# Kernel optimization log

Hardware: AMD Instinct MI355X
Metric: run time of the kernel (lower is better)

The kernel has to match this reference:

```python
import jax, jax.numpy as jnp
import numpy as np

EPS = 0.1
N_ITERS = 20


def setup_inputs() -> dict:
    key = jax.random.key(0)
    D = jax.random.uniform(key, (32, 1024, 1024), dtype=jnp.float32)
    return {"D": D}


def reference(D) -> jnp.ndarray:
    log_K0 = -D / EPS  # [B, N, M]

    def body(_, log_K):
        # row normalization (over dim 2), then column normalization (over dim 1)
        log_K = log_K - jax.scipy.special.logsumexp(log_K, axis=2, keepdims=True)
        log_K = log_K - jax.scipy.special.logsumexp(log_K, axis=1, keepdims=True)
        return log_K

    log_K = jax.lax.fori_loop(0, N_ITERS, body, log_K0)
    # transport plan weighted cost, summed per batch, then mean over batch
    return jnp.mean(jnp.sum(jnp.exp(log_K) * D, axis=(1, 2)))
```

## Files before the change

kernel.cpp:

```cpp
#include <hip/hip_runtime.h>

#define BATCH 32
#define NMAT 1024
#define NPB 64
#define RPB (NMAT / NPB)
#define NBLOCKS (BATCH * NPB)
#define N_ITERS 20
#define SHIFT 5.0f

typedef _Float16 h8 __attribute__((ext_vector_type(8)));

__device__ __forceinline__ float wave_allsum(float s) {
#pragma unroll
    for (int off = 1; off < 64; off <<= 1) s += __shfl_xor(s, off, 64);
    return s;
}

__device__ __forceinline__ float4 f4add(float4 a, float4 b) {
    return make_float4(a.x + b.x, a.y + b.y, a.z + b.z, a.w + b.w);
}

__global__ __launch_bounds__(256) void pass1_build(const float* __restrict__ D,
                                                   _Float16* __restrict__ E,
                                                   float* __restrict__ P) {
    const int j = blockIdx.x;
    const int row0 = j * RPB;
    const int wave = threadIdx.x >> 6, lane = threadIdx.x & 63;

    float4 acc[4] = {make_float4(0,0,0,0), make_float4(0,0,0,0),
                     make_float4(0,0,0,0), make_float4(0,0,0,0)};

#pragma unroll
    for (int i = 0; i < RPB / 4; ++i) {
        const int r = row0 + wave + (i << 2);
        const float4* Dr = (const float4*)(D + ((size_t)r << 10));
        h8* Er = (h8*)(E + ((size_t)r << 10));
        float t[16];
        float s = 0.f;
#pragma unroll
        for (int k2 = 0; k2 < 2; ++k2) {
            const int c = lane + (k2 << 6);
            float4 d0 = Dr[2 * c], d1 = Dr[2 * c + 1];
            float* tv = t + (k2 << 3);
            tv[0] = __expf(fmaf(d0.x, -10.f, SHIFT));
            tv[1] = __expf(fmaf(d0.y, -10.f, SHIFT));
            tv[2] = __expf(fmaf(d0.z, -10.f, SHIFT));
            tv[3] = __expf(fmaf(d0.w, -10.f, SHIFT));
            tv[4] = __expf(fmaf(d1.x, -10.f, SHIFT));
            tv[5] = __expf(fmaf(d1.y, -10.f, SHIFT));
            tv[6] = __expf(fmaf(d1.z, -10.f, SHIFT));
            tv[7] = __expf(fmaf(d1.w, -10.f, SHIFT));
            h8 o;
#pragma unroll
            for (int q = 0; q < 8; ++q) o[q] = (_Float16)tv[q];
            Er[c] = o;
#pragma unroll
            for (int q = 0; q < 8; ++q) s += tv[q];
        }
        s = wave_allsum(s);
        const float rs = __builtin_amdgcn_rcpf(s);
#pragma unroll
        for (int k2 = 0; k2 < 2; ++k2) {
            float* tv = t + (k2 << 3);
            float4* a0 = &acc[k2 << 1];
            a0[0].x = fmaf(tv[0], rs, a0[0].x);
            a0[0].y = fmaf(tv[1], rs, a0[0].y);
            a0[0].z = fmaf(tv[2], rs, a0[0].z);
            a0[0].w = fmaf(tv[3], rs, a0[0].w);
            a0[1].x = fmaf(tv[4], rs, a0[1].x);
            a0[1].y = fmaf(tv[5], rs, a0[1].y);
            a0[1].z = fmaf(tv[6], rs, a0[1].z);
            a0[1].w = fmaf(tv[7], rs, a0[1].w);
        }
    }

    __shared__ float4 pc[4][256];
#pragma unroll
    for (int k2 = 0; k2 < 2; ++k2) {
        const int c = lane + (k2 << 6);
        pc[wave][2 * c]     = acc[k2 << 1];
        pc[wave][2 * c + 1] = acc[(k2 << 1) + 1];
    }
    __syncthreads();
    const int i = threadIdx.x;
    float4 o = f4add(f4add(pc[0][i], pc[1][i]), f4add(pc[2][i], pc[3][i]));
    ((float4*)(P + ((size_t)j << 10)))[i] = o;
}

template <bool LAST>
__global__ __launch_bounds__(256) void pass_iter(const _Float16* __restrict__ E,
                                                 const float* __restrict__ ev_in,
                                                 float* __restrict__ P,
                                                 float* __restrict__ Q,
                                                 float* __restrict__ out) {
    const int j = blockIdx.x;
    const int row0 = j * RPB;
    const int b = row0 >> 10;
    const int wave = threadIdx.x >> 6, lane = threadIdx.x & 63;

    float ev[16];
    {
        const float4* evb = (const float4*)(ev_in + (b << 10));
#pragma unroll
        for (int k2 = 0; k2 < 2; ++k2) {
            const int c = lane + (k2 << 6);
            float4 e0 = evb[2 * c], e1 = evb[2 * c + 1];
            float* e = ev + (k2 << 3);
            e[0] = e0.x; e[1] = e0.y; e[2] = e0.z; e[3] = e0.w;
            e[4] = e1.x; e[5] = e1.y; e[6] = e1.z; e[7] = e1.w;
        }
    }

    float4 acc[4] = {make_float4(0,0,0,0), make_float4(0,0,0,0),
                     make_float4(0,0,0,0), make_float4(0,0,0,0)};
    float4 qacc[4] = {make_float4(0,0,0,0), make_float4(0,0,0,0),
                      make_float4(0,0,0,0), make_float4(0,0,0,0)};

#pragma unroll
    for (int i = 0; i < RPB / 4; ++i) {
        const int r = row0 + wave + (i << 2);
        const h8* Er = (const h8*)(E + ((size_t)r << 10));
        h8 h0 = Er[lane], h1 = Er[lane + 64];
        float t[16];
#pragma unroll
        for (int q = 0; q < 8; ++q) { t[q] = (float)h0[q]; t[8 + q] = (float)h1[q]; }
        float s = 0.f;
#pragma unroll
        for (int q = 0; q < 16; ++q) s = fmaf(t[q], ev[q], s);
        s = wave_allsum(s);
        const float rs = __builtin_amdgcn_rcpf(s);
#pragma unroll
        for (int k2 = 0; k2 < 2; ++k2) {
            float* tv = t + (k2 << 3);
            float4* a0 = &acc[k2 << 1];
            a0[0].x = fmaf(tv[0], rs, a0[0].x);
            a0[0].y = fmaf(tv[1], rs, a0[0].y);
            a0[0].z = fmaf(tv[2], rs, a0[0].z);
            a0[0].w = fmaf(tv[3], rs, a0[0].w);
            a0[1].x = fmaf(tv[4], rs, a0[1].x);
            a0[1].y = fmaf(tv[5], rs, a0[1].y);
            a0[1].z = fmaf(tv[6], rs, a0[1].z);
            a0[1].w = fmaf(tv[7], rs, a0[1].w);
        }
        if (LAST) {
#pragma unroll
            for (int k2 = 0; k2 < 2; ++k2) {
                float* tv = t + (k2 << 3);
                float4* q0 = &qacc[k2 << 1];
                float w[8];
#pragma unroll
                for (int q = 0; q < 8; ++q) {
                    const float d = (SHIFT - __logf(tv[q])) * 0.1f;
                    w[q] = tv[q] * d;
                }
                q0[0].x = fmaf(w[0], rs, q0[0].x);
                q0[0].y = fmaf(w[1], rs, q0[0].y);
                q0[0].z = fmaf(w[2], rs, q0[0].z);
                q0[0].w = fmaf(w[3], rs, q0[0].w);
                q0[1].x = fmaf(w[4], rs, q0[1].x);
                q0[1].y = fmaf(w[5], rs, q0[1].y);
                q0[1].z = fmaf(w[6], rs, q0[1].z);
                q0[1].w = fmaf(w[7], rs, q0[1].w);
            }
        }
    }

    __shared__ float4 pc[4][256];
#pragma unroll
    for (int k2 = 0; k2 < 2; ++k2) {
        const int c = lane + (k2 << 6);
        pc[wave][2 * c]     = acc[k2 << 1];
        pc[wave][2 * c + 1] = acc[(k2 << 1) + 1];
    }
    __syncthreads();
    {
        const int i = threadIdx.x;
        float4 o = f4add(f4add(pc[0][i], pc[1][i]), f4add(pc[2][i], pc[3][i]));
        ((float4*)(P + ((size_t)j << 10)))[i] = o;
    }
    if (LAST) {
        __syncthreads();
#pragma unroll
        for (int k2 = 0; k2 < 2; ++k2) {
            const int c = lane + (k2 << 6);
            pc[wave][2 * c]     = qacc[k2 << 1];
            pc[wave][2 * c + 1] = qacc[(k2 << 1) + 1];
        }
        __syncthreads();
        const int i = threadIdx.x;
        float4 o = f4add(f4add(pc[0][i], pc[1][i]), f4add(pc[2][i], pc[3][i]));
        ((float4*)(Q + ((size_t)j << 10)))[i] = o;
        if (j == 0 && threadIdx.x == 0) out[0] = 0.f;
    }
}

__global__ __launch_bounds__(256) void reduce_ev(const float* __restrict__ P,
                                                 float* __restrict__ ev) {
    int g = blockIdx.x * 256 + threadIdx.x;
    int b = g >> 10, m = g & 1023;
    const float* Pb = P + (((size_t)b * NPB) << 10) + m;
    float s = 0.f;
#pragma unroll 8
    for (int jj = 0; jj < NPB; ++jj) s += Pb[(size_t)jj << 10];
    ev[g] = 1.0f / s;
}

__global__ __launch_bounds__(256) void loss_final(const float* __restrict__ P,
                                                  const float* __restrict__ Q,
                                                  float* __restrict__ out) {
    int g = blockIdx.x * 256 + threadIdx.x;
    int b = g >> 10, m = g & 1023;
    const float* Pb = P + (((size_t)b * NPB) << 10) + m;
    const float* Qb = Q + (((size_t)b * NPB) << 10) + m;
    float s = 0.f, q = 0.f;
#pragma unroll 8
    for (int jj = 0; jj < NPB; ++jj) {
        s += Pb[(size_t)jj << 10];
        q += Qb[(size_t)jj << 10];
    }
    float c = q / s;
    c = wave_allsum(c);
    __shared__ float sm[4];
    int wave = threadIdx.x >> 6, lane = threadIdx.x & 63;
    if (lane == 0) sm[wave] = c;
    __syncthreads();
    if (threadIdx.x == 0)
        atomicAdd(out, (sm[0] + sm[1] + sm[2] + sm[3]) * (1.0f / (float)BATCH));
}

extern "C" void kernel_launch(void* const* d_in, const int* in_sizes, int n_in,
                              void* d_out, int out_size, void* d_ws, size_t ws_size,
                              hipStream_t stream) {
    const float* D = (const float*)d_in[0];
    float* out = (float*)d_out;

    float* ev = (float*)d_ws;
    float* P  = ev + BATCH * NMAT;
    float* Q  = P + (size_t)NBLOCKS * NMAT;
    _Float16* E = (_Float16*)(Q + (size_t)NBLOCKS * NMAT);

    pass1_build<<<NBLOCKS, 256, 0, stream>>>(D, E, P);
    for (int t = 1; t < N_ITERS - 1; ++t) {
        reduce_ev<<<(BATCH * NMAT) / 256, 256, 0, stream>>>(P, ev);
        pass_iter<false><<<NBLOCKS, 256, 0, stream>>>(E, ev, P, Q, out);
    }
    reduce_ev<<<(BATCH * NMAT) / 256, 256, 0, stream>>>(P, ev);
    pass_iter<true><<<NBLOCKS, 256, 0, stream>>>(E, ev, P, Q, out);
    loss_final<<<(BATCH * NMAT) / 256, 256, 0, stream>>>(P, Q, out);
}
```

Before: 560.1 us.

## Fuse Sinkhorn iterations into persistent kernel with on-chip E and grid barriers

Replaces the per-iteration launches of pass_iter and reduce_ev with one persistent kernel of 256 blocks of 1024 threads. Each block keeps its 128-row slab of the fp16 kernel matrix on chip, five rows per wave in registers and three in LDS, so the matrix is not re-read from HBM each iteration. Iterations are separated by atomic-counter grid barriers, and column scalings are reduced from double-buffered partials. The risks are register and LDS pressure, a deadlock if all 256 blocks are not co-resident, and the cost of the barrier spins.

```diff
diff --git a/kernel.cpp b/kernel.cpp
--- a/kernel.cpp
+++ b/kernel.cpp
@@ -2,9 +2,11 @@
 
 #define BATCH 32
 #define NMAT 1024
-#define NPB 64
-#define RPB (NMAT / NPB)
-#define NBLOCKS (BATCH * NPB)
+#define NBLK 256
+#define NWAVE 16
+#define ROWS_PW 8
+#define REG_ROWS 5
+#define LDS_ROWS 3
 #define N_ITERS 20
 #define SHIFT 5.0f
 
@@ -20,212 +22,196 @@
     return make_float4(a.x + b.x, a.y + b.y, a.z + b.z, a.w + b.w);
 }
 
-__global__ __launch_bounds__(256) void pass1_build(const float* __restrict__ D,
-                                                   _Float16* __restrict__ E,
-                                                   float* __restrict__ P) {
-    const int j = blockIdx.x;
-    const int row0 = j * RPB;
-    const int wave = threadIdx.x >> 6, lane = threadIdx.x & 63;
-
-    float4 acc[4] = {make_float4(0,0,0,0), make_float4(0,0,0,0),
-                     make_float4(0,0,0,0), make_float4(0,0,0,0)};
-
-#pragma unroll
-    for (int i = 0; i < RPB / 4; ++i) {
-        const int r = row0 + wave + (i << 2);
-        const float4* Dr = (const float4*)(D + ((size_t)r << 10));
-        h8* Er = (h8*)(E + ((size_t)r << 10));
-        float t[16];
-        float s = 0.f;
-#pragma unroll
-        for (int k2 = 0; k2 < 2; ++k2) {
-            const int c = lane + (k2 << 6);
-            float4 d0 = Dr[2 * c], d1 = Dr[2 * c + 1];
-            float* tv = t + (k2 << 3);
-            tv[0] = __expf(fmaf(d0.x, -10.f, SHIFT));
-            tv[1] = __expf(fmaf(d0.y, -10.f, SHIFT));
-            tv[2] = __expf(fmaf(d0.z, -10.f, SHIFT));
-            tv[3] = __expf(fmaf(d0.w, -10.f, SHIFT));
-            tv[4] = __expf(fmaf(d1.x, -10.f, SHIFT));
-            tv[5] = __expf(fmaf(d1.y, -10.f, SHIFT));
-            tv[6] = __expf(fmaf(d1.z, -10.f, SHIFT));
-            tv[7] = __expf(fmaf(d1.w, -10.f, SHIFT));
-            h8 o;
-#pragma unroll
-            for (int q = 0; q < 8; ++q) o[q] = (_Float16)tv[q];
-            Er[c] = o;
-#pragma unroll
-            for (int q = 0; q < 8; ++q) s += tv[q];
-        }
-        s = wave_allsum(s);
-        const float rs = __builtin_amdgcn_rcpf(s);
-#pragma unroll
-        for (int k2 = 0; k2 < 2; ++k2) {
-            float* tv = t + (k2 << 3);
-            float4* a0 = &acc[k2 << 1];
-            a0[0].x = fmaf(tv[0], rs, a0[0].x);
-            a0[0].y = fmaf(tv[1], rs, a0[0].y);
-            a0[0].z = fmaf(tv[2], rs, a0[0].z);
-            a0[0].w = fmaf(tv[3], rs, a0[0].w);
-            a0[1].x = fmaf(tv[4], rs, a0[1].x);
-            a0[1].y = fmaf(tv[5], rs, a0[1].y);
-            a0[1].z = fmaf(tv[6], rs, a0[1].z);
-            a0[1].w = fmaf(tv[7], rs, a0[1].w);
-        }
-    }
-
-    __shared__ float4 pc[4][256];
-#pragma unroll
-    for (int k2 = 0; k2 < 2; ++k2) {
-        const int c = lane + (k2 << 6);
-        pc[wave][2 * c]     = acc[k2 << 1];
-        pc[wave][2 * c + 1] = acc[(k2 << 1) + 1];
-    }
-    __syncthreads();
-    const int i = threadIdx.x;
-    float4 o = f4add(f4add(pc[0][i], pc[1][i]), f4add(pc[2][i], pc[3][i]));
-    ((float4*)(P + ((size_t)j << 10)))[i] = o;
-}
-
-template <bool LAST>
-__global__ __launch_bounds__(256) void pass_iter(const _Float16* __restrict__ E,
-                                                 const float* __restrict__ ev_in,
-                                                 float* __restrict__ P,
-                                                 float* __restrict__ Q,
-                                                 float* __restrict__ out) {
-    const int j = blockIdx.x;
-    const int row0 = j * RPB;
-    const int b = row0 >> 10;
-    const int wave = threadIdx.x >> 6, lane = threadIdx.x & 63;
-
-    float ev[16];
-    {
-        const float4* evb = (const float4*)(ev_in + (b << 10));
-#pragma unroll
-        for (int k2 = 0; k2 < 2; ++k2) {
-            const int c = lane + (k2 << 6);
-            float4 e0 = evb[2 * c], e1 = evb[2 * c + 1];
-            float* e = ev + (k2 << 3);
-            e[0] = e0.x; e[1] = e0.y; e[2] = e0.z; e[3] = e0.w;
-            e[4] = e1.x; e[5] = e1.y; e[6] = e1.z; e[7] = e1.w;
-        }
-    }
-
-    float4 acc[4] = {make_float4(0,0,0,0), make_float4(0,0,0,0),
-                     make_float4(0,0,0,0), make_float4(0,0,0,0)};
-    float4 qacc[4] = {make_float4(0,0,0,0), make_float4(0,0,0,0),
-                      make_float4(0,0,0,0), make_float4(0,0,0,0)};
-
-#pragma unroll
-    for (int i = 0; i < RPB / 4; ++i) {
-        const int r = row0 + wave + (i << 2);
-        const h8* Er = (const h8*)(E + ((size_t)r << 10));
-        h8 h0 = Er[lane], h1 = Er[lane + 64];
-        float t[16];
-#pragma unroll
-        for (int q = 0; q < 8; ++q) { t[q] = (float)h0[q]; t[8 + q] = (float)h1[q]; }
-        float s = 0.f;
-#pragma unroll
-        for (int q = 0; q < 16; ++q) s = fmaf(t[q], ev[q], s);
-        s = wave_allsum(s);
-        const float rs = __builtin_amdgcn_rcpf(s);
-#pragma unroll
-        for (int k2 = 0; k2 < 2; ++k2) {
-            float* tv = t + (k2 << 3);
-            float4* a0 = &acc[k2 << 1];
-            a0[0].x = fmaf(tv[0], rs, a0[0].x);
-            a0[0].y = fmaf(tv[1], rs, a0[0].y);
-            a0[0].z = fmaf(tv[2], rs, a0[0].z);
-            a0[0].w = fmaf(tv[3], rs, a0[0].w);
-            a0[1].x = fmaf(tv[4], rs, a0[1].x);
-            a0[1].y = fmaf(tv[5], rs, a0[1].y);
-            a0[1].z = fmaf(tv[6], rs, a0[1].z);
-            a0[1].w = fmaf(tv[7], rs, a0[1].w);
-        }
-        if (LAST) {
-#pragma unroll
-            for (int k2 = 0; k2 < 2; ++k2) {
-                float* tv = t + (k2 << 3);
-                float4* q0 = &qacc[k2 << 1];
-                float w[8];
-#pragma unroll
-                for (int q = 0; q < 8; ++q) {
-                    const float d = (SHIFT - __logf(tv[q])) * 0.1f;
-                    w[q] = tv[q] * d;
-                }
-                q0[0].x = fmaf(w[0], rs, q0[0].x);
-                q0[0].y = fmaf(w[1], rs, q0[0].y);
-                q0[0].z = fmaf(w[2], rs, q0[0].z);
-                q0[0].w = fmaf(w[3], rs, q0[0].w);
-                q0[1].x = fmaf(w[4], rs, q0[1].x);
-                q0[1].y = fmaf(w[5], rs, q0[1].y);
-                q0[1].z = fmaf(w[6], rs, q0[1].z);
-                q0[1].w = fmaf(w[7], rs, q0[1].w);
-            }
-        }
-    }
-
-    __shared__ float4 pc[4][256];
-#pragma unroll
-    for (int k2 = 0; k2 < 2; ++k2) {
-        const int c = lane + (k2 << 6);
-        pc[wave][2 * c]     = acc[k2 << 1];
-        pc[wave][2 * c + 1] = acc[(k2 << 1) + 1];
-    }
-    __syncthreads();
-    {
-        const int i = threadIdx.x;
-        float4 o = f4add(f4add(pc[0][i], pc[1][i]), f4add(pc[2][i], pc[3][i]));
-        ((float4*)(P + ((size_t)j << 10)))[i] = o;
-    }
-    if (LAST) {
+__global__ void init_ctr(unsigned* __restrict__ ctr) { ctr[threadIdx.x] = 0u; }
+
+__device__ __forceinline__ float stage_colsum(const float* acc, float4* sbuf,
+                                              int wave, int lane, int tid) {
+    const int w4 = wave & 3;
+    float4 mine[4];
+#pragma unroll
+    for (int h = 0; h < 4; ++h) {
+        const float* a = acc + ((h >> 1) << 3) + ((h & 1) << 2);
+        mine[h] = make_float4(a[0], a[1], a[2], a[3]);
+    }
+    __syncthreads();
+    if (wave < 4) {
+#pragma unroll
+        for (int h = 0; h < 4; ++h) sbuf[(w4 << 8) + (h << 6) + lane] = mine[h];
+    }
+    __syncthreads();
+#pragma unroll
+    for (int g = 1; g < 4; ++g) {
+        if ((wave >> 2) == g) {
+#pragma unroll
+            for (int h = 0; h < 4; ++h) {
+                const int idx = (w4 << 8) + (h << 6) + lane;
+                sbuf[idx] = f4add(sbuf[idx], mine[h]);
+            }
+        }
         __syncthreads();
-#pragma unroll
-        for (int k2 = 0; k2 < 2; ++k2) {
-            const int c = lane + (k2 << 6);
-            pc[wave][2 * c]     = qacc[k2 << 1];
-            pc[wave][2 * c + 1] = qacc[(k2 << 1) + 1];
-        }
-        __syncthreads();
-        const int i = threadIdx.x;
-        float4 o = f4add(f4add(pc[0][i], pc[1][i]), f4add(pc[2][i], pc[3][i]));
-        ((float4*)(Q + ((size_t)j << 10)))[i] = o;
-        if (j == 0 && threadIdx.x == 0) out[0] = 0.f;
-    }
-}
-
-__global__ __launch_bounds__(256) void reduce_ev(const float* __restrict__ P,
-                                                 float* __restrict__ ev) {
-    int g = blockIdx.x * 256 + threadIdx.x;
-    int b = g >> 10, m = g & 1023;
-    const float* Pb = P + (((size_t)b * NPB) << 10) + m;
-    float s = 0.f;
-#pragma unroll 8
-    for (int jj = 0; jj < NPB; ++jj) s += Pb[(size_t)jj << 10];
-    ev[g] = 1.0f / s;
-}
-
-__global__ __launch_bounds__(256) void loss_final(const float* __restrict__ P,
-                                                  const float* __restrict__ Q,
-                                                  float* __restrict__ out) {
-    int g = blockIdx.x * 256 + threadIdx.x;
-    int b = g >> 10, m = g & 1023;
-    const float* Pb = P + (((size_t)b * NPB) << 10) + m;
-    const float* Qb = Q + (((size_t)b * NPB) << 10) + m;
-    float s = 0.f, q = 0.f;
-#pragma unroll 8
-    for (int jj = 0; jj < NPB; ++jj) {
-        s += Pb[(size_t)jj << 10];
-        q += Qb[(size_t)jj << 10];
-    }
-    float c = q / s;
-    c = wave_allsum(c);
-    __shared__ float sm[4];
-    int wave = threadIdx.x >> 6, lane = threadIdx.x & 63;
-    if (lane == 0) sm[wave] = c;
-    __syncthreads();
-    if (threadIdx.x == 0)
-        atomicAdd(out, (sm[0] + sm[1] + sm[2] + sm[3]) * (1.0f / (float)BATCH));
+    }
+    const int rem = tid & 511, lt = rem >> 3, ut = rem & 7;
+    const int ht = ((tid >> 9) << 1) + (ut >> 2), rt = ut & 3;
+    const float* bf = (const float*)sbuf;
+    float cs = 0.f;
+#pragma unroll
+    for (int w = 0; w < 4; ++w) cs += bf[(((w << 8) + (ht << 6) + lt) << 2) + rt];
+    return cs;
+}
+
+__device__ __forceinline__ void grid_barrier(unsigned* c, int tid) {
+    __syncthreads();
+    if (tid == 0) {
+        __threadfence();
+        __hip_atomic_fetch_add(c, 1u, __ATOMIC_RELEASE, __HIP_MEMORY_SCOPE_AGENT);
+        int guard = 0;
+        while (__hip_atomic_load(c, __ATOMIC_RELAXED, __HIP_MEMORY_SCOPE_AGENT) < NBLK &&
+               guard < (1 << 24)) {
+            __builtin_amdgcn_s_sleep(2);
+            ++guard;
+        }
+        (void)__hip_atomic_load(c, __ATOMIC_ACQUIRE, __HIP_MEMORY_SCOPE_AGENT);
+    }
+    __syncthreads();
+}
+
+__global__ void __launch_bounds__(1024)
+sinkhorn_persist(const float* __restrict__ D, float* __restrict__ Pg,
+                 float* __restrict__ Qg, unsigned* __restrict__ ctr,
+                 float* __restrict__ out) {
+    __shared__ __align__(16) _Float16 eL[NWAVE * LDS_ROWS][NMAT];
+    __shared__ float4 sbuf[1024];
+    __shared__ float4 evb4[NMAT / 4];
+    float* evb = (float*)evb4;
+
+    const int b = blockIdx.x;
+    const int bb = b >> 3, slab = b & 7;
+    const int tid = threadIdx.x;
+    const int wave = tid >> 6, lane = tid & 63;
+    const size_t rbase = ((size_t)bb << 10) + (slab << 7) + (wave << 3);
+
+    h8 er[REG_ROWS][2];
+    float evr[16];
+    float colacc[16], qacc[16];
+
+#pragma unroll 1
+    for (int it = 0; it < N_ITERS; ++it) {
+        const bool last = (it == N_ITERS - 1);
+#pragma unroll
+        for (int q = 0; q < 16; ++q) colacc[q] = 0.f;
+        if (last) {
+#pragma unroll
+            for (int q = 0; q < 16; ++q) qacc[q] = 0.f;
+        }
+
+        if (it == 0) {
+#pragma unroll
+            for (int rr = 0; rr < ROWS_PW; ++rr) {
+                const float4* D4 = (const float4*)(D + ((rbase + rr) << 10));
+                float t[16];
+#pragma unroll
+                for (int k2 = 0; k2 < 2; ++k2) {
+                    const int c = lane + (k2 << 6);
+                    float4 d0 = D4[2 * c], d1 = D4[2 * c + 1];
+                    float* tv = t + (k2 << 3);
+                    tv[0] = __expf(fmaf(d0.x, -10.f, SHIFT));
+                    tv[1] = __expf(fmaf(d0.y, -10.f, SHIFT));
+                    tv[2] = __expf(fmaf(d0.z, -10.f, SHIFT));
+                    tv[3] = __expf(fmaf(d0.w, -10.f, SHIFT));
+                    tv[4] = __expf(fmaf(d1.x, -10.f, SHIFT));
+                    tv[5] = __expf(fmaf(d1.y, -10.f, SHIFT));
+                    tv[6] = __expf(fmaf(d1.z, -10.f, SHIFT));
+                    tv[7] = __expf(fmaf(d1.w, -10.f, SHIFT));
+                    h8 o;
+#pragma unroll
+                    for (int q = 0; q < 8; ++q) o[q] = (_Float16)tv[q];
+                    if (rr < REG_ROWS) er[rr][k2] = o;
+                    else ((h8*)eL[wave * LDS_ROWS + rr - REG_ROWS])[c] = o;
+                }
+                float s = 0.f;
+#pragma unroll
+                for (int q = 0; q < 16; ++q) s += t[q];
+                s = wave_allsum(s);
+                const float rs = __builtin_amdgcn_rcpf(s);
+#pragma unroll
+                for (int q = 0; q < 16; ++q) colacc[q] = fmaf(t[q], rs, colacc[q]);
+            }
+        } else {
+            {
+#pragma unroll
+                for (int h = 0; h < 4; ++h) {
+                    float4 e = evb4[(h << 6) + lane];
+                    float* ev = evr + ((h >> 1) << 3) + ((h & 1) << 2);
+                    ev[0] = e.x; ev[1] = e.y; ev[2] = e.z; ev[3] = e.w;
+                }
+            }
+#pragma unroll
+            for (int rr = 0; rr < ROWS_PW; ++rr) {
+                h8 h0, h1;
+                if (rr < REG_ROWS) { h0 = er[rr][0]; h1 = er[rr][1]; }
+                else {
+                    const h8* Er = (const h8*)eL[wave * LDS_ROWS + rr - REG_ROWS];
+                    h0 = Er[lane]; h1 = Er[lane + 64];
+                }
+                float t[16];
+#pragma unroll
+                for (int q = 0; q < 8; ++q) { t[q] = (float)h0[q]; t[8 + q] = (float)h1[q]; }
+                float s = 0.f;
+#pragma unroll
+                for (int q = 0; q < 16; ++q) s = fmaf(t[q], evr[q], s);
+                s = wave_allsum(s);
+                const float rs = __builtin_amdgcn_rcpf(s);
+#pragma unroll
+                for (int q = 0; q < 16; ++q) colacc[q] = fmaf(t[q], rs, colacc[q]);
+                if (last) {
+#pragma unroll
+                    for (int q = 0; q < 16; ++q) {
+                        const float dd = (SHIFT - __logf(t[q])) * 0.1f;
+                        qacc[q] = fmaf(t[q] * dd, rs, qacc[q]);
+                    }
+                }
+            }
+        }
+
+        const int par = it & 1;
+        const float cs = stage_colsum(colacc, sbuf, wave, lane, tid);
+        Pg[((par * NBLK + b) << 10) + tid] = cs;
+        if (last) {
+            const float qs = stage_colsum(qacc, sbuf, wave, lane, tid);
+            Qg[(b << 10) + tid] = qs;
+            if (b == 0 && tid == 0) out[0] = 0.f;
+        }
+
+        grid_barrier(&ctr[it], tid);
+
+        if (!last) {
+            const float* Pb = Pg + ((par * NBLK + (bb << 3)) << 10) + tid;
+            float s8 = 0.f;
+#pragma unroll
+            for (int j = 0; j < 8; ++j) s8 += Pb[j << 10];
+            const float evv = 1.0f / s8;
+            const int rem = tid & 511, lt = rem >> 3, ut = rem & 7;
+            const int ht = ((tid >> 9) << 1) + (ut >> 2), rt = ut & 3;
+            evb[(((ht << 6) + lt) << 2) + rt] = evv;
+            __syncthreads();
+        } else if (slab == 0) {
+            const float* Pb = Pg + ((par * NBLK + (bb << 3)) << 10) + tid;
+            const float* Qb = Qg + (((bb << 3)) << 10) + tid;
+            float s8 = 0.f, q8 = 0.f;
+#pragma unroll
+            for (int j = 0; j < 8; ++j) { s8 += Pb[j << 10]; q8 += Qb[j << 10]; }
+            float c = q8 / s8;
+            c = wave_allsum(c);
+            if (lane == 0) ((float*)sbuf)[wave] = c;
+            __syncthreads();
+            if (tid == 0) {
+                float tot = 0.f;
+#pragma unroll
+                for (int w = 0; w < NWAVE; ++w) tot += ((float*)sbuf)[w];
+                atomicAdd(out, tot * (1.0f / (float)BATCH));
+            }
+        }
+    }
 }
 
 extern "C" void kernel_launch(void* const* d_in, const int* in_sizes, int n_in,
@@ -234,17 +220,10 @@
     const float* D = (const float*)d_in[0];
     float* out = (float*)d_out;
 
-    float* ev = (float*)d_ws;
-    float* P  = ev + BATCH * NMAT;
-    float* Q  = P + (size_t)NBLOCKS * NMAT;
-    _Float16* E = (_Float16*)(Q + (size_t)NBLOCKS * NMAT);
-
-    pass1_build<<<NBLOCKS, 256, 0, stream>>>(D, E, P);
-    for (int t = 1; t < N_ITERS - 1; ++t) {
-        reduce_ev<<<(BATCH * NMAT) / 256, 256, 0, stream>>>(P, ev);
-        pass_iter<false><<<NBLOCKS, 256, 0, stream>>>(E, ev, P, Q, out);
-    }
-    reduce_ev<<<(BATCH * NMAT) / 256, 256, 0, stream>>>(P, ev);
-    pass_iter<true><<<NBLOCKS, 256, 0, stream>>>(E, ev, P, Q, out);
-    loss_final<<<(BATCH * NMAT) / 256, 256, 0, stream>>>(P, Q, out);
-}
+    unsigned* ctr = (unsigned*)d_ws;
+    float* Pg = (float*)((char*)d_ws + 1024);
+    float* Qg = Pg + 2 * NBLK * NMAT;
+
+    init_ctr<<<1, 64, 0, stream>>>(ctr);
+    sinkhorn_persist<<<NBLK, NWAVE * 64, 0, stream>>>(D, Pg, Qg, ctr, out);
+}
```

Result: slower. 1.323 ms (+136.1%).
